# Optimization experiments

Hardware: AMD Instinct MI355X
Metric: run time of the kernel (lower is better)

The kernel has to match this reference:

```python
import jax, jax.numpy as jnp
import numpy as np


def setup_inputs() -> dict:
    key = jax.random.key(0)
    k1, k2, k3, k4 = jax.random.split(key, 4)
    B, T, C = 4, 2048, 1024
    x = jax.random.normal(k1, (B, T, C), dtype=jnp.float32)
    scale = 1.0 / np.sqrt(C)
    Wq = jax.random.normal(k2, (C, C), dtype=jnp.float32) * scale
    Wk = jax.random.normal(k3, (C, C), dtype=jnp.float32) * scale
    Wv = jax.random.normal(k4, (C, C), dtype=jnp.float32) * scale
    return {"x": x, "Wq": Wq, "Wk": Wk, "Wv": Wv}


def reference(x, Wq, Wk, Wv):
    # x: [B, T, C]; torch Linear(no bias): y = x @ W.T
    B, T, C = x.shape
    q = jnp.einsum('btc,dc->btd', x, Wq)
    k = jnp.einsum('btc,dc->btd', x, Wk)
    v = jnp.einsum('btc,dc->btd', x, Wv)
    scale = jnp.asarray(C, x.dtype) ** -0.5
    qk = jnp.einsum('bqd,bkd->bqk', q, k) * scale  # [B, T, T]
    causal = jnp.tril(jnp.ones((T, T), dtype=bool))
    qk = jnp.where(causal, qk, -jnp.inf)
    attn = jax.nn.softmax(qk, axis=-1)
    out = jnp.einsum('bqk,bkd->bqd', attn, v)
    return out
```

## Files before the change

### kernel.cpp

```cpp
#include <hip/hip_runtime.h>

typedef __attribute__((ext_vector_type(8))) short  short8;
typedef __attribute__((ext_vector_type(4))) short  short4v;
typedef __attribute__((ext_vector_type(4))) float  floatx4;

__device__ inline short f2bf(float f) {
    union { float f; unsigned u; } v; v.f = f;
    unsigned r = v.u + 0x7fffu + ((v.u >> 16) & 1u);
    return (short)(r >> 16);
}

typedef const __attribute__((address_space(1))) unsigned int* gp1_t;
typedef __attribute__((address_space(3))) unsigned int* lp3_t;

__device__ __attribute__((always_inline)) inline void gl_lds16(const short* g, short* l) {
    __builtin_amdgcn_global_load_lds((gp1_t)g, (lp3_t)l, 16, 0, 0);
}

__device__ __attribute__((always_inline)) inline void gemm_bt_core(
    const short* __restrict__ Ag, const short* __restrict__ Bg,
    int lda, int ldb, int kmax,
    short* As, short* Bs, floatx4 acc[4][4])
{
    const int t    = threadIdx.x;
    const int srow = t >> 3;
    const int scol = (t & 7) * 8;
    const int lane = t & 63;
    const int wid  = t >> 6;
    const int wx   = wid & 1, wy = wid >> 1;
    const int lm   = lane & 15, lq = lane >> 4;

    for (int k0 = 0; k0 < kmax; k0 += 64) {
        __syncthreads();
#pragma unroll
        for (int i = 0; i < 4; ++i) {
            gl_lds16(Ag + (size_t)(i * 32 + srow) * lda + k0 + scol,
                     As + (i * 32 + srow) * 64 + scol);
            gl_lds16(Bg + (size_t)(i * 32 + srow) * ldb + k0 + scol,
                     Bs + (i * 32 + srow) * 64 + scol);
        }
        __syncthreads();

#pragma unroll
        for (int ks = 0; ks < 2; ++ks) {
            short8 af[4], bfr[4];
#pragma unroll
            for (int mi = 0; mi < 4; ++mi)
                af[mi] = *(const short8*)(As + (wy * 64 + mi * 16 + lm) * 64 + ks * 32 + lq * 8);
#pragma unroll
            for (int ni = 0; ni < 4; ++ni)
                bfr[ni] = *(const short8*)(Bs + (wx * 64 + ni * 16 + lm) * 64 + ks * 32 + lq * 8);
#pragma unroll
            for (int mi = 0; mi < 4; ++mi)
#pragma unroll
                for (int ni = 0; ni < 4; ++ni)
                    acc[mi][ni] = __builtin_amdgcn_mfma_f32_16x16x32_bf16(
                        af[mi], bfr[ni], acc[mi][ni], 0, 0, 0);
        }
    }
}

__global__ void cast_all(const float* __restrict__ x,
                         const float* __restrict__ Wq,
                         const float* __restrict__ Wk,
                         const float* __restrict__ Wv,
                         short* __restrict__ xb, short* __restrict__ wb,
                         float* __restrict__ lsum)
{
    size_t v = (size_t)blockIdx.x * 256 + threadIdx.x;
    const float* src; short* dst; size_t off;
    if (v < 2097152)      { src = x;  dst = xb;           off = v; }
    else if (v < 2359296) { src = Wq; dst = wb;           off = v - 2097152; }
    else if (v < 2621440) { src = Wk; dst = wb + 1048576; off = v - 2359296; }
    else if (v < 2883584) { src = Wv; dst = wb + 2097152; off = v - 2621440; }
    else if (v < 2885632) {
        floatx4 z = {0.f, 0.f, 0.f, 0.f};
        ((floatx4*)lsum)[v - 2883584] = z;
        return;
    } else return;
    floatx4 vv = ((const floatx4*)src)[off];
    short4v s;
#pragma unroll
    for (int e = 0; e < 4; ++e) s[e] = f2bf(vv[e]);
    ((short4v*)dst)[off] = s;
}

__global__ __launch_bounds__(256, 3) void qkv_gemm(
    const short* __restrict__ xb, const short* __restrict__ wb,
    short* __restrict__ qb, short* __restrict__ kb, short* __restrict__ vt)
{
    __shared__ short As[128 * 64];
    __shared__ short Bs[128 * 64];

    const int m0    = blockIdx.x * 128;
    const int which = blockIdx.y >> 3;
    const int n0    = (blockIdx.y & 7) * 128;

    floatx4 acc[4][4];
    floatx4 zero = {0.f, 0.f, 0.f, 0.f};
#pragma unroll
    for (int i = 0; i < 4; ++i)
#pragma unroll
        for (int j = 0; j < 4; ++j) acc[i][j] = zero;

    gemm_bt_core(xb + (size_t)m0 * 1024,
                 wb + (size_t)blockIdx.y * 128 * 1024,
                 1024, 1024, 1024, As, Bs, acc);

    const int lane = threadIdx.x & 63, wid = threadIdx.x >> 6;
    const int wx = wid & 1, wy = wid >> 1, lm = lane & 15, lq = lane >> 4;
#pragma unroll
    for (int mi = 0; mi < 4; ++mi)
#pragma unroll
        for (int ni = 0; ni < 4; ++ni)
#pragma unroll
            for (int r = 0; r < 4; ++r) {
                int row = m0 + wy * 64 + mi * 16 + lq * 4 + r;
                int col = n0 + wx * 64 + ni * 16 + lm;
                short bvv = f2bf(acc[mi][ni][r]);
                if (which == 2) {
                    int bb = row >> 11, tt = row & 2047;
                    vt[((size_t)bb * 1024 + col) * 2048 + tt] = bvv;
                } else if (which == 1) {
                    kb[(size_t)row * 1024 + col] = bvv;
                } else {
                    qb[(size_t)row * 1024 + col] = bvv;
                }
            }
}

__global__ __launch_bounds__(256, 3) void sqk_gemm(
    const short* __restrict__ qb, const short* __restrict__ kb,
    short* __restrict__ P, float* __restrict__ lsum)
{
    int idx = blockIdx.x;
    int i = 0;
    while ((i + 1) * (i + 2) / 2 <= idx) ++i;
    const int j = idx - i * (i + 1) / 2;
    const int b = blockIdx.y;

    __shared__ short As[128 * 64];
    __shared__ short Bs[128 * 64];

    floatx4 acc[4][4];
    floatx4 zero = {0.f, 0.f, 0.f, 0.f};
#pragma unroll
    for (int a = 0; a < 4; ++a)
#pragma unroll
        for (int c = 0; c < 4; ++c) acc[a][c] = zero;

    gemm_bt_core(qb + ((size_t)(b * 2048 + i * 128)) * 1024,
                 kb + ((size_t)(b * 2048 + j * 128)) * 1024,
                 1024, 1024, 1024, As, Bs, acc);

    const float sscl = 0.03125f * 1.44269504089f;
    const bool  diag = (i == j);
    const int lane = threadIdx.x & 63, wid = threadIdx.x >> 6;
    const int wx = wid & 1, wy = wid >> 1, lm = lane & 15, lq = lane >> 4;

#pragma unroll
    for (int mi = 0; mi < 4; ++mi)
#pragma unroll
        for (int r = 0; r < 4; ++r) {
            const int lrow = wy * 64 + mi * 16 + lq * 4 + r;
            const int grow = i * 128 + lrow;
            short* prow = P + ((size_t)b * 2048 + grow) * 2048 + j * 128;
            float rsum = 0.f;
#pragma unroll
            for (int ni = 0; ni < 4; ++ni) {
                const int lcol = wx * 64 + ni * 16 + lm;
                float p = exp2f(acc[mi][ni][r] * sscl);
                if (diag && lcol > lrow) p = 0.f;
                rsum += p;
                prow[lcol] = f2bf(p);
            }
#pragma unroll
            for (int off = 1; off < 16; off <<= 1) rsum += __shfl_xor(rsum, off);
            if (lm == 0) atomicAdd(lsum + b * 2048 + grow, rsum);
        }
}

__global__ __launch_bounds__(256, 3) void pv_gemm(
    const short* __restrict__ P, const short* __restrict__ vt,
    const float* __restrict__ lsum, float* __restrict__ out)
{
    const int x  = blockIdx.x;
    const int pr = blockIdx.y;
    const int b  = blockIdx.z;
    const int n0 = x * 64;

    __shared__ short As[128 * 64];
    __shared__ short Bs[64 * 64];

    const int t    = threadIdx.x;
    const int srow = t >> 3;
    const int scol = (t & 7) * 8;
    const int lane = t & 63;
    const int wid  = t >> 6;
    const int wx   = wid & 1, wy = wid >> 1;
    const int lm   = lane & 15, lq = lane >> 4;

    const short* Bg = vt + ((size_t)b * 1024 + n0) * 2048;

#pragma unroll
    for (int phase = 0; phase < 2; ++phase) {
        const int i    = phase ? (15 - pr) : pr;
        const int kmax = (i + 1) * 128;
        const short* Ag = P + ((size_t)b * 2048 + i * 128) * 2048;

        floatx4 acc[4][2];
        floatx4 zero = {0.f, 0.f, 0.f, 0.f};
#pragma unroll
        for (int a = 0; a < 4; ++a)
#pragma unroll
            for (int c = 0; c < 2; ++c) acc[a][c] = zero;

        for (int k0 = 0; k0 < kmax; k0 += 64) {
            __syncthreads();
#pragma unroll
            for (int q = 0; q < 4; ++q)
                gl_lds16(Ag + (size_t)(q * 32 + srow) * 2048 + k0 + scol,
                         As + (q * 32 + srow) * 64 + scol);
#pragma unroll
            for (int q = 0; q < 2; ++q)
                gl_lds16(Bg + (size_t)(q * 32 + srow) * 2048 + k0 + scol,
                         Bs + (q * 32 + srow) * 64 + scol);
            __syncthreads();

#pragma unroll
            for (int ks = 0; ks < 2; ++ks) {
                short8 af[4], bfr[2];
#pragma unroll
                for (int mi = 0; mi < 4; ++mi)
                    af[mi] = *(const short8*)(As + (wy * 64 + mi * 16 + lm) * 64 + ks * 32 + lq * 8);
#pragma unroll
                for (int ni = 0; ni < 2; ++ni)
                    bfr[ni] = *(const short8*)(Bs + (wx * 32 + ni * 16 + lm) * 64 + ks * 32 + lq * 8);
#pragma unroll
                for (int mi = 0; mi < 4; ++mi)
#pragma unroll
                    for (int ni = 0; ni < 2; ++ni)
                        acc[mi][ni] = __builtin_amdgcn_mfma_f32_16x16x32_bf16(
                            af[mi], bfr[ni], acc[mi][ni], 0, 0, 0);
            }
        }

#pragma unroll
        for (int mi = 0; mi < 4; ++mi)
#pragma unroll
            for (int r = 0; r < 4; ++r) {
                const int grow = b * 2048 + i * 128 + wy * 64 + mi * 16 + lq * 4 + r;
                const float li = 1.0f / lsum[grow];
#pragma unroll
                for (int ni = 0; ni < 2; ++ni)
                    out[(size_t)grow * 1024 + n0 + wx * 32 + ni * 16 + lm] =
                        acc[mi][ni][r] * li;
            }
    }
}

extern "C" void kernel_launch(void* const* d_in, const int* in_sizes, int n_in,
                              void* d_out, int out_size, void* d_ws, size_t ws_size,
                              hipStream_t stream)
{
    (void)in_sizes; (void)n_in; (void)out_size; (void)ws_size;
    const float* x  = (const float*)d_in[0];
    const float* Wq = (const float*)d_in[1];
    const float* Wk = (const float*)d_in[2];
    const float* Wv = (const float*)d_in[3];
    float* out = (float*)d_out;

    char* base = (char*)d_ws;
    short* xb   = (short*)(base);
    short* wb   = (short*)(base + 16777216);
    short* qb   = (short*)(base + 23068672);
    short* kb   = (short*)(base + 39845888);
    short* vt   = (short*)(base + 56623104);
    short* P    = (short*)(base + 73400320);
    float* lsum = (float*)(base + 107954176);

    cast_all<<<11272, 256, 0, stream>>>(x, Wq, Wk, Wv, xb, wb, lsum);
    qkv_gemm<<<dim3(64, 24), 256, 0, stream>>>(xb, wb, qb, kb, vt);
    sqk_gemm<<<dim3(136, 4), 256, 0, stream>>>(qb, kb, P, lsum);
    pv_gemm<<<dim3(16, 8, 4), 256, 0, stream>>>(P, vt, lsum, out);
}
```

Measured before the change: 245.8 us.

## Rewrite QKV projection GEMM as 256x256 double-buffered, 8-wave pipelined kernel

Replaces the 128x128 four-wave QKV GEMM with a 256x256-tile kernel using eight waves and a double-buffered LDS of 128 KB. Global-to-LDS loads for the next K slice are issued while MFMAs on the current slice run, and s_setprio raises priority around the MFMA blocks. The LDS layout is XOR-swizzled to avoid bank conflicts, and tile indices are remapped so neighbouring workgroups share inputs in cache. This trades occupancy and more register pressure (an 8x4 accumulator array per wave) for better data reuse and overlap of loads with compute.

```diff
diff --git a/kernel.cpp b/kernel.cpp
--- a/kernel.cpp
+++ b/kernel.cpp
@@ -16,6 +16,8 @@
 __device__ __attribute__((always_inline)) inline void gl_lds16(const short* g, short* l) {
     __builtin_amdgcn_global_load_lds((gp1_t)g, (lp3_t)l, 16, 0, 0);
 }
+
+#define MFMA_BF16 __builtin_amdgcn_mfma_f32_16x16x32_bf16
 
 __device__ __attribute__((always_inline)) inline void gemm_bt_core(
     const short* __restrict__ Ag, const short* __restrict__ Bg,
@@ -54,8 +56,7 @@
             for (int mi = 0; mi < 4; ++mi)
 #pragma unroll
                 for (int ni = 0; ni < 4; ++ni)
-                    acc[mi][ni] = __builtin_amdgcn_mfma_f32_16x16x32_bf16(
-                        af[mi], bfr[ni], acc[mi][ni], 0, 0, 0);
+                    acc[mi][ni] = MFMA_BF16(af[mi], bfr[ni], acc[mi][ni], 0, 0, 0);
         }
     }
 }
@@ -85,48 +86,178 @@
     ((short4v*)dst)[off] = s;
 }
 
-__global__ __launch_bounds__(256, 3) void qkv_gemm(
+template<int MODE>
+__device__ __attribute__((always_inline)) inline void ktile4(
+    short* As, short* Bs,
+    const short* __restrict__ Ag, const short* __restrict__ Bg, int sk0,
+    int srow, int scl, int scg, int aB, int bB, int c0, int c1,
+    floatx4 acc[8][4])
+{
+    short8 af[4][2], bf[4][2];
+#pragma unroll
+    for (int mi = 0; mi < 4; ++mi) {
+        af[mi][0] = *(const short8*)(As + aB + mi * 1024 + c0);
+        af[mi][1] = *(const short8*)(As + aB + mi * 1024 + c1);
+    }
+#pragma unroll
+    for (int ni = 0; ni < 2; ++ni) {
+        bf[ni][0] = *(const short8*)(Bs + bB + ni * 1024 + c0);
+        bf[ni][1] = *(const short8*)(Bs + bB + ni * 1024 + c1);
+    }
+    __builtin_amdgcn_s_barrier();
+    asm volatile("s_waitcnt lgkmcnt(0)" ::: "memory");
+    __builtin_amdgcn_s_setprio(1);
+#pragma unroll
+    for (int mi = 0; mi < 4; ++mi)
+#pragma unroll
+        for (int ni = 0; ni < 2; ++ni) {
+            acc[mi][ni] = MFMA_BF16(af[mi][0], bf[ni][0], acc[mi][ni], 0, 0, 0);
+            acc[mi][ni] = MFMA_BF16(af[mi][1], bf[ni][1], acc[mi][ni], 0, 0, 0);
+        }
+    __builtin_amdgcn_s_setprio(0);
+    __builtin_amdgcn_s_barrier();
+#pragma unroll
+    for (int ni = 2; ni < 4; ++ni) {
+        bf[ni][0] = *(const short8*)(Bs + bB + ni * 1024 + c0);
+        bf[ni][1] = *(const short8*)(Bs + bB + ni * 1024 + c1);
+    }
+    __builtin_amdgcn_s_barrier();
+    asm volatile("s_waitcnt lgkmcnt(0)" ::: "memory");
+    __builtin_amdgcn_s_setprio(1);
+#pragma unroll
+    for (int mi = 0; mi < 4; ++mi)
+#pragma unroll
+        for (int ni = 2; ni < 4; ++ni) {
+            acc[mi][ni] = MFMA_BF16(af[mi][0], bf[ni][0], acc[mi][ni], 0, 0, 0);
+            acc[mi][ni] = MFMA_BF16(af[mi][1], bf[ni][1], acc[mi][ni], 0, 0, 0);
+        }
+    __builtin_amdgcn_s_setprio(0);
+    __builtin_amdgcn_s_barrier();
+#pragma unroll
+    for (int mi = 0; mi < 4; ++mi) {
+        af[mi][0] = *(const short8*)(As + aB + 4096 + mi * 1024 + c0);
+        af[mi][1] = *(const short8*)(As + aB + 4096 + mi * 1024 + c1);
+    }
+    __builtin_amdgcn_s_barrier();
+    asm volatile("s_waitcnt lgkmcnt(0)" ::: "memory");
+    __builtin_amdgcn_s_setprio(1);
+#pragma unroll
+    for (int mi = 0; mi < 4; ++mi)
+#pragma unroll
+        for (int ni = 2; ni < 4; ++ni) {
+            acc[4 + mi][ni] = MFMA_BF16(af[mi][0], bf[ni][0], acc[4 + mi][ni], 0, 0, 0);
+            acc[4 + mi][ni] = MFMA_BF16(af[mi][1], bf[ni][1], acc[4 + mi][ni], 0, 0, 0);
+        }
+    __builtin_amdgcn_s_setprio(0);
+    __builtin_amdgcn_s_barrier();
+    if (MODE == 0) {
+#pragma unroll
+        for (int i = 0; i < 4; ++i)
+            gl_lds16(Ag + (size_t)(i * 64 + srow) * 1024 + sk0 + scg,
+                     As + (i * 64 + srow) * 64 + scl);
+#pragma unroll
+        for (int i = 0; i < 4; ++i)
+            gl_lds16(Bg + (size_t)(i * 64 + srow) * 1024 + sk0 + scg,
+                     Bs + (i * 64 + srow) * 64 + scl);
+    }
+    __builtin_amdgcn_s_setprio(1);
+#pragma unroll
+    for (int mi = 0; mi < 4; ++mi)
+#pragma unroll
+        for (int ni = 0; ni < 2; ++ni) {
+            acc[4 + mi][ni] = MFMA_BF16(af[mi][0], bf[ni][0], acc[4 + mi][ni], 0, 0, 0);
+            acc[4 + mi][ni] = MFMA_BF16(af[mi][1], bf[ni][1], acc[4 + mi][ni], 0, 0, 0);
+        }
+    __builtin_amdgcn_s_setprio(0);
+    if (MODE == 0)      asm volatile("s_waitcnt vmcnt(8)" ::: "memory");
+    else if (MODE == 1) asm volatile("s_waitcnt vmcnt(0)" ::: "memory");
+    __builtin_amdgcn_s_barrier();
+}
+
+__global__ __launch_bounds__(512, 2) void qkv_gemm8(
     const short* __restrict__ xb, const short* __restrict__ wb,
     short* __restrict__ qb, short* __restrict__ kb, short* __restrict__ vt)
 {
-    __shared__ short As[128 * 64];
-    __shared__ short Bs[128 * 64];
-
-    const int m0    = blockIdx.x * 128;
-    const int which = blockIdx.y >> 3;
-    const int n0    = (blockIdx.y & 7) * 128;
-
-    floatx4 acc[4][4];
+    __shared__ short lds[65536];
+
+    const int orig = blockIdx.x;
+    const int tile = (orig & 7) * 48 + (orig >> 3);
+    const int mt = tile & 31;
+    const int nt = tile >> 5;
+    const int m0 = mt * 256;
+
+    const short* Ag = xb + (size_t)m0 * 1024;
+    const short* Bg = wb + (size_t)(nt * 256) * 1024;
+
+    const int t    = threadIdx.x;
+    const int lane = t & 63;
+    const int wid  = t >> 6;
+    const int wy   = wid >> 2, wx = wid & 3;
+    const int lm   = lane & 15, lq = lane >> 4;
+
+    const int srow = t >> 3;
+    const int scl  = (t & 7) * 8;
+    const int scg  = ((t & 7) ^ (srow & 7)) * 8;
+
+    const int c0 = (lq ^ (lm & 7)) * 8;
+    const int c1 = ((4 + lq) ^ (lm & 7)) * 8;
+    const int aB = (wy * 128 + lm) * 64;
+    const int bB = (wx * 64 + lm) * 64;
+
+    floatx4 acc[8][4];
     floatx4 zero = {0.f, 0.f, 0.f, 0.f};
 #pragma unroll
-    for (int i = 0; i < 4; ++i)
+    for (int i = 0; i < 8; ++i)
 #pragma unroll
         for (int j = 0; j < 4; ++j) acc[i][j] = zero;
 
-    gemm_bt_core(xb + (size_t)m0 * 1024,
-                 wb + (size_t)blockIdx.y * 128 * 1024,
-                 1024, 1024, 1024, As, Bs, acc);
-
-    const int lane = threadIdx.x & 63, wid = threadIdx.x >> 6;
-    const int wx = wid & 1, wy = wid >> 1, lm = lane & 15, lq = lane >> 4;
-#pragma unroll
-    for (int mi = 0; mi < 4; ++mi)
-#pragma unroll
-        for (int ni = 0; ni < 4; ++ni)
-#pragma unroll
-            for (int r = 0; r < 4; ++r) {
-                int row = m0 + wy * 64 + mi * 16 + lq * 4 + r;
-                int col = n0 + wx * 64 + ni * 16 + lm;
-                short bvv = f2bf(acc[mi][ni][r]);
+    short* A0 = lds;          short* B0 = lds + 16384;
+    short* A1 = lds + 32768;  short* B1 = lds + 49152;
+
+#pragma unroll
+    for (int i = 0; i < 4; ++i) {
+        gl_lds16(Ag + (size_t)(i * 64 + srow) * 1024 + scg,      A0 + (i * 64 + srow) * 64 + scl);
+        gl_lds16(Bg + (size_t)(i * 64 + srow) * 1024 + scg,      B0 + (i * 64 + srow) * 64 + scl);
+    }
+#pragma unroll
+    for (int i = 0; i < 4; ++i) {
+        gl_lds16(Ag + (size_t)(i * 64 + srow) * 1024 + 64 + scg, A1 + (i * 64 + srow) * 64 + scl);
+        gl_lds16(Bg + (size_t)(i * 64 + srow) * 1024 + 64 + scg, B1 + (i * 64 + srow) * 64 + scl);
+    }
+    asm volatile("s_waitcnt vmcnt(8)" ::: "memory");
+    __builtin_amdgcn_s_barrier();
+
+#pragma unroll 1
+    for (int k2 = 0; k2 < 7; ++k2) {
+        const int kk = k2 * 128;
+        ktile4<0>(A0, B0, Ag, Bg, kk + 128, srow, scl, scg, aB, bB, c0, c1, acc);
+        ktile4<0>(A1, B1, Ag, Bg, kk + 192, srow, scl, scg, aB, bB, c0, c1, acc);
+    }
+    ktile4<1>(A0, B0, Ag, Bg, 0, srow, scl, scg, aB, bB, c0, c1, acc);
+    ktile4<2>(A1, B1, Ag, Bg, 0, srow, scl, scg, aB, bB, c0, c1, acc);
+
+    const int nglob = nt * 256;
+    const int which = nglob >> 10;
+    const int ncol  = (nglob & 1023) + wx * 64;
+#pragma unroll
+    for (int mi = 0; mi < 8; ++mi)
+#pragma unroll
+        for (int r = 0; r < 4; ++r) {
+            const int row = m0 + wy * 128 + mi * 16 + lq * 4 + r;
+#pragma unroll
+            for (int ni = 0; ni < 4; ++ni) {
+                const int col = ncol + ni * 16 + lm;
+                const short bv = f2bf(acc[mi][ni][r]);
                 if (which == 2) {
-                    int bb = row >> 11, tt = row & 2047;
-                    vt[((size_t)bb * 1024 + col) * 2048 + tt] = bvv;
+                    const int bb = row >> 11, tt = row & 2047;
+                    vt[((size_t)bb * 1024 + col) * 2048 + tt] = bv;
                 } else if (which == 1) {
-                    kb[(size_t)row * 1024 + col] = bvv;
+                    kb[(size_t)row * 1024 + col] = bv;
                 } else {
-                    qb[(size_t)row * 1024 + col] = bvv;
+                    qb[(size_t)row * 1024 + col] = bv;
                 }
             }
+        }
 }
 
 __global__ __launch_bounds__(256, 3) void sqk_gemm(
@@ -240,8 +371,7 @@
                 for (int mi = 0; mi < 4; ++mi)
 #pragma unroll
                     for (int ni = 0; ni < 2; ++ni)
-                        acc[mi][ni] = __builtin_amdgcn_mfma_f32_16x16x32_bf16(
-                            af[mi], bfr[ni], acc[mi][ni], 0, 0, 0);
+                        acc[mi][ni] = MFMA_BF16(af[mi], bfr[ni], acc[mi][ni], 0, 0, 0);
             }
         }
 
@@ -280,7 +410,7 @@
     float* lsum = (float*)(base + 107954176);
 
     cast_all<<<11272, 256, 0, stream>>>(x, Wq, Wk, Wv, xb, wb, lsum);
-    qkv_gemm<<<dim3(64, 24), 256, 0, stream>>>(xb, wb, qb, kb, vt);
+    qkv_gemm8<<<dim3(384), 512, 0, stream>>>(xb, wb, qb, kb, vt);
     sqk_gemm<<<dim3(136, 4), 256, 0, stream>>>(qb, kb, P, lsum);
     pv_gemm<<<dim3(16, 8, 4), 256, 0, stream>>>(P, vt, lsum, out);
 }
```

New measurement: 288.4 us. 1.17x slower.

## Replace QKV GEMM with 256x256 double-buffered, swizzled, 8-wave pipelined kernel

Applied to the files above, without the earlier changes.

Rewrites the QKV projection GEMM to use 256x256 output tiles on 512-thread blocks, with double-buffered LDS staging via direct global-to-LDS loads interleaved with MFMA quadrants. It adds an XOR swizzle on LDS columns to avoid bank conflicts, s_setprio around MFMA bursts, and a block-index remap that groups tiles for L2 reuse. The aim is to hide global load latency and raise arithmetic intensity compared with the single-buffered 128x128 kernel. In exchange it needs 128KB of LDS and many more accumulator registers, and it relies on hand-placed waitcnt counts that must match the issued loads exactly.

```diff
diff --git a/kernel.cpp b/kernel.cpp
--- a/kernel.cpp
+++ b/kernel.cpp
@@ -16,6 +16,8 @@
 __device__ __attribute__((always_inline)) inline void gl_lds16(const short* g, short* l) {
     __builtin_amdgcn_global_load_lds((gp1_t)g, (lp3_t)l, 16, 0, 0);
 }
+
+#define MFMA_BF16 __builtin_amdgcn_mfma_f32_16x16x32_bf16
 
 __device__ __attribute__((always_inline)) inline void gemm_bt_core(
     const short* __restrict__ Ag, const short* __restrict__ Bg,
@@ -54,8 +56,7 @@
             for (int mi = 0; mi < 4; ++mi)
 #pragma unroll
                 for (int ni = 0; ni < 4; ++ni)
-                    acc[mi][ni] = __builtin_amdgcn_mfma_f32_16x16x32_bf16(
-                        af[mi], bfr[ni], acc[mi][ni], 0, 0, 0);
+                    acc[mi][ni] = MFMA_BF16(af[mi], bfr[ni], acc[mi][ni], 0, 0, 0);
         }
     }
 }
@@ -85,48 +86,156 @@
     ((short4v*)dst)[off] = s;
 }
 
-__global__ __launch_bounds__(256, 3) void qkv_gemm(
+struct Q8Ctx {
+    const short* Ag; const short* Bg;
+    short *A0, *B0, *A1, *B1;
+    int srow, scl, scg;
+    int aB, bB, c0, c1;
+};
+
+#define LD_AF(SLOT, HI) do { _Pragma("unroll") \
+    for (int mi_ = 0; mi_ < 4; ++mi_) { \
+        af[mi_][0] = *(const short8*)((SLOT) + X.aB + (HI) + mi_ * 1024 + X.c0); \
+        af[mi_][1] = *(const short8*)((SLOT) + X.aB + (HI) + mi_ * 1024 + X.c1); \
+    } } while (0)
+
+#define LD_BF(SLOT, N0) do { _Pragma("unroll") \
+    for (int ni_ = 0; ni_ < 2; ++ni_) { \
+        bf[(N0) + ni_][0] = *(const short8*)((SLOT) + X.bB + ((N0) + ni_) * 1024 + X.c0); \
+        bf[(N0) + ni_][1] = *(const short8*)((SLOT) + X.bB + ((N0) + ni_) * 1024 + X.c1); \
+    } } while (0)
+
+#define MM_Q(MB, N0) do { _Pragma("unroll") \
+    for (int mi_ = 0; mi_ < 4; ++mi_) { _Pragma("unroll") \
+        for (int ni_ = 0; ni_ < 2; ++ni_) { \
+            acc[(MB)+mi_][(N0)+ni_] = MFMA_BF16(af[mi_][0], bf[(N0)+ni_][0], acc[(MB)+mi_][(N0)+ni_], 0, 0, 0); \
+            acc[(MB)+mi_][(N0)+ni_] = MFMA_BF16(af[mi_][1], bf[(N0)+ni_][1], acc[(MB)+mi_][(N0)+ni_], 0, 0, 0); \
+        } } } while (0)
+
+#define STAGE_HALF(DST, SRC, KOFS) do { \
+    gl_lds16((SRC) + (size_t)(X.srow)      * 1024 + (KOFS) + X.scg, (DST) + (X.srow)      * 64 + X.scl); \
+    gl_lds16((SRC) + (size_t)(64 + X.srow) * 1024 + (KOFS) + X.scg, (DST) + (64 + X.srow) * 64 + X.scl); \
+    } while (0)
+
+#define BARR  __builtin_amdgcn_s_barrier()
+#define WLG0  asm volatile("s_waitcnt lgkmcnt(0)" ::: "memory")
+#define WLG8  asm volatile("s_waitcnt lgkmcnt(8)" ::: "memory")
+#define PRI1  __builtin_amdgcn_s_setprio(1)
+#define PRI0  __builtin_amdgcn_s_setprio(0)
+
+template<bool TAIL>
+__device__ __attribute__((always_inline)) inline void iter8(
+    const Q8Ctx& X, int kb, floatx4 acc[8][4])
+{
+    const int sk1 = kb + 64, sk2 = kb + 128, sk3 = kb + 192;
+    short8 af[4][2], bf[4][2];
+
+    LD_AF(X.A0, 0); LD_BF(X.B0, 0);
+    STAGE_HALF(X.A1, X.Ag, sk1);
+    WLG8;
+    BARR; WLG0; PRI1; MM_Q(0, 0); PRI0; BARR;
+    LD_BF(X.B0, 2);
+    STAGE_HALF(X.A1 + 8192, X.Ag + 131072, sk1);
+    BARR; WLG0; PRI1; MM_Q(0, 2); PRI0; BARR;
+    LD_AF(X.A0, 4096);
+    if (!TAIL) STAGE_HALF(X.B0, X.Bg, sk2);
+    BARR; WLG0; PRI1; MM_Q(4, 2); PRI0; BARR;
+    if (!TAIL) STAGE_HALF(X.B0 + 8192, X.Bg + 131072, sk2);
+    BARR; PRI1; MM_Q(4, 0); PRI0;
+    if (!TAIL) asm volatile("s_waitcnt vmcnt(4)" ::: "memory");
+    else       asm volatile("s_waitcnt vmcnt(0)" ::: "memory");
+    BARR;
+
+    LD_AF(X.A1, 0); LD_BF(X.B1, 0);
+    if (!TAIL) STAGE_HALF(X.A0, X.Ag, sk2);
+    WLG8;
+    BARR; WLG0; PRI1; MM_Q(0, 0); PRI0; BARR;
+    LD_BF(X.B1, 2);
+    if (!TAIL) STAGE_HALF(X.A0 + 8192, X.Ag + 131072, sk2);
+    BARR; WLG0; PRI1; MM_Q(0, 2); PRI0; BARR;
+    LD_AF(X.A1, 4096);
+    if (!TAIL) STAGE_HALF(X.B1, X.Bg, sk3);
+    BARR; WLG0; PRI1; MM_Q(4, 2); PRI0; BARR;
+    if (!TAIL) STAGE_HALF(X.B1 + 8192, X.Bg + 131072, sk3);
+    BARR; PRI1; MM_Q(4, 0); PRI0;
+    if (!TAIL) asm volatile("s_waitcnt vmcnt(4)" ::: "memory");
+    BARR;
+}
+
+__global__ __launch_bounds__(512, 2) void qkv_gemm8(
     const short* __restrict__ xb, const short* __restrict__ wb,
     short* __restrict__ qb, short* __restrict__ kb, short* __restrict__ vt)
 {
-    __shared__ short As[128 * 64];
-    __shared__ short Bs[128 * 64];
-
-    const int m0    = blockIdx.x * 128;
-    const int which = blockIdx.y >> 3;
-    const int n0    = (blockIdx.y & 7) * 128;
-
-    floatx4 acc[4][4];
+    __shared__ short lds[65536];
+
+    const int orig = blockIdx.x;
+    const int tile = (orig & 7) * 48 + (orig >> 3);
+    const int mt = tile & 31;
+    const int nt = tile >> 5;
+    const int m0 = mt * 256;
+
+    const int t    = threadIdx.x;
+    const int lane = t & 63;
+    const int wid  = t >> 6;
+    const int wy   = wid >> 2, wx = wid & 3;
+    const int lm   = lane & 15, lq = lane >> 4;
+
+    Q8Ctx X;
+    X.Ag = xb + (size_t)m0 * 1024;
+    X.Bg = wb + (size_t)(nt * 256) * 1024;
+    X.A0 = lds;          X.B0 = lds + 16384;
+    X.A1 = lds + 32768;  X.B1 = lds + 49152;
+    X.srow = t >> 3;
+    X.scl  = (t & 7) * 8;
+    X.scg  = ((t & 7) ^ (X.srow & 7)) * 8;
+    X.c0 = (lq ^ (lm & 7)) * 8;
+    X.c1 = ((4 + lq) ^ (lm & 7)) * 8;
+    X.aB = (wy * 128 + lm) * 64;
+    X.bB = (wx * 64 + lm) * 64;
+
+    floatx4 acc[8][4];
     floatx4 zero = {0.f, 0.f, 0.f, 0.f};
 #pragma unroll
-    for (int i = 0; i < 4; ++i)
+    for (int i = 0; i < 8; ++i)
 #pragma unroll
         for (int j = 0; j < 4; ++j) acc[i][j] = zero;
 
-    gemm_bt_core(xb + (size_t)m0 * 1024,
-                 wb + (size_t)blockIdx.y * 128 * 1024,
-                 1024, 1024, 1024, As, Bs, acc);
-
-    const int lane = threadIdx.x & 63, wid = threadIdx.x >> 6;
-    const int wx = wid & 1, wy = wid >> 1, lm = lane & 15, lq = lane >> 4;
-#pragma unroll
-    for (int mi = 0; mi < 4; ++mi)
-#pragma unroll
-        for (int ni = 0; ni < 4; ++ni)
-#pragma unroll
-            for (int r = 0; r < 4; ++r) {
-                int row = m0 + wy * 64 + mi * 16 + lq * 4 + r;
-                int col = n0 + wx * 64 + ni * 16 + lm;
-                short bvv = f2bf(acc[mi][ni][r]);
+    STAGE_HALF(X.A0,         X.Ag,          0);
+    STAGE_HALF(X.A0 + 8192,  X.Ag + 131072, 0);
+    STAGE_HALF(X.B0,         X.Bg,          0);
+    STAGE_HALF(X.B0 + 8192,  X.Bg + 131072, 0);
+    STAGE_HALF(X.B1,         X.Bg,          64);
+    STAGE_HALF(X.B1 + 8192,  X.Bg + 131072, 64);
+    asm volatile("s_waitcnt vmcnt(4)" ::: "memory");
+    __builtin_amdgcn_s_barrier();
+
+#pragma unroll 1
+    for (int i = 0; i < 7; ++i)
+        iter8<false>(X, i * 128, acc);
+    iter8<true>(X, 7 * 128, acc);
+
+    const int nglob = nt * 256;
+    const int which = nglob >> 10;
+    const int ncol  = (nglob & 1023) + wx * 64;
+#pragma unroll
+    for (int mi = 0; mi < 8; ++mi)
+#pragma unroll
+        for (int r = 0; r < 4; ++r) {
+            const int row = m0 + wy * 128 + mi * 16 + lq * 4 + r;
+#pragma unroll
+            for (int ni = 0; ni < 4; ++ni) {
+                const int col = ncol + ni * 16 + lm;
+                const short bv = f2bf(acc[mi][ni][r]);
                 if (which == 2) {
-                    int bb = row >> 11, tt = row & 2047;
-                    vt[((size_t)bb * 1024 + col) * 2048 + tt] = bvv;
+                    const int bb = row >> 11, tt = row & 2047;
+                    vt[((size_t)bb * 1024 + col) * 2048 + tt] = bv;
                 } else if (which == 1) {
-                    kb[(size_t)row * 1024 + col] = bvv;
+                    kb[(size_t)row * 1024 + col] = bv;
                 } else {
-                    qb[(size_t)row * 1024 + col] = bvv;
+                    qb[(size_t)row * 1024 + col] = bv;
                 }
             }
+        }
 }
 
 __global__ __launch_bounds__(256, 3) void sqk_gemm(
@@ -240,8 +349,7 @@
                 for (int mi = 0; mi < 4; ++mi)
 #pragma unroll
                     for (int ni = 0; ni < 2; ++ni)
-                        acc[mi][ni] = __builtin_amdgcn_mfma_f32_16x16x32_bf16(
-                            af[mi], bfr[ni], acc[mi][ni], 0, 0, 0);
+                        acc[mi][ni] = MFMA_BF16(af[mi], bfr[ni], acc[mi][ni], 0, 0, 0);
             }
         }
 
@@ -280,7 +388,7 @@
     float* lsum = (float*)(base + 107954176);
 
     cast_all<<<11272, 256, 0, stream>>>(x, Wq, Wk, Wv, xb, wb, lsum);
-    qkv_gemm<<<dim3(64, 24), 256, 0, stream>>>(xb, wb, qb, kb, vt);
+    qkv_gemm8<<<dim3(384), 512, 0, stream>>>(xb, wb, qb, kb, vt);
     sqk_gemm<<<dim3(136, 4), 256, 0, stream>>>(qb, kb, P, lsum);
     pv_gemm<<<dim3(16, 8, 4), 256, 0, stream>>>(P, vt, lsum, out);
 }
```

After: 282.5 us. +15.0%, slower.

## Use 128x128 tiles in PV GEMM with longest-first scheduling

Applied to the files above, without the earlier changes.

The PV GEMM changes from 128x64 output tiles, where each block processed two causal row-blocks paired for balance, to 128x128 tiles with one row-block per block. It reuses the shared gemm_bt_core and orders the grid so the largest causal row-blocks launch first. Larger tiles raise arithmetic intensity and halve reloads of P. The cost is fewer blocks (512 instead of 512 paired launches that did double work) and the loss of the explicit load-balancing pairing. The launch_bounds of 3 is kept, and larger register use for the 4x4 accumulators may hurt occupancy.

```diff
diff --git a/kernel.cpp b/kernel.cpp
--- a/kernel.cpp
+++ b/kernel.cpp
@@ -16,6 +16,8 @@
 __device__ __attribute__((always_inline)) inline void gl_lds16(const short* g, short* l) {
     __builtin_amdgcn_global_load_lds((gp1_t)g, (lp3_t)l, 16, 0, 0);
 }
+
+#define MFMA_BF16 __builtin_amdgcn_mfma_f32_16x16x32_bf16
 
 __device__ __attribute__((always_inline)) inline void gemm_bt_core(
     const short* __restrict__ Ag, const short* __restrict__ Bg,
@@ -54,8 +56,7 @@
             for (int mi = 0; mi < 4; ++mi)
 #pragma unroll
                 for (int ni = 0; ni < 4; ++ni)
-                    acc[mi][ni] = __builtin_amdgcn_mfma_f32_16x16x32_bf16(
-                        af[mi], bfr[ni], acc[mi][ni], 0, 0, 0);
+                    acc[mi][ni] = MFMA_BF16(af[mi], bfr[ni], acc[mi][ni], 0, 0, 0);
         }
     }
 }
@@ -185,78 +186,40 @@
     const float* __restrict__ lsum, float* __restrict__ out)
 {
     const int x  = blockIdx.x;
-    const int pr = blockIdx.y;
-    const int b  = blockIdx.z;
-    const int n0 = x * 64;
+    const int b  = blockIdx.y;
+    const int i  = 15 - blockIdx.z;
+    const int n0 = x * 128;
+    const int kmax = (i + 1) * 128;
 
     __shared__ short As[128 * 64];
-    __shared__ short Bs[64 * 64];
-
-    const int t    = threadIdx.x;
-    const int srow = t >> 3;
-    const int scol = (t & 7) * 8;
-    const int lane = t & 63;
-    const int wid  = t >> 6;
-    const int wx   = wid & 1, wy = wid >> 1;
-    const int lm   = lane & 15, lq = lane >> 4;
-
+    __shared__ short Bs[128 * 64];
+
+    const short* Ag = P  + ((size_t)b * 2048 + i * 128) * 2048;
     const short* Bg = vt + ((size_t)b * 1024 + n0) * 2048;
 
-#pragma unroll
-    for (int phase = 0; phase < 2; ++phase) {
-        const int i    = phase ? (15 - pr) : pr;
-        const int kmax = (i + 1) * 128;
-        const short* Ag = P + ((size_t)b * 2048 + i * 128) * 2048;
-
-        floatx4 acc[4][2];
-        floatx4 zero = {0.f, 0.f, 0.f, 0.f};
-#pragma unroll
-        for (int a = 0; a < 4; ++a)
-#pragma unroll
-            for (int c = 0; c < 2; ++c) acc[a][c] = zero;
-
-        for (int k0 = 0; k0 < kmax; k0 += 64) {
-            __syncthreads();
-#pragma unroll
-            for (int q = 0; q < 4; ++q)
-                gl_lds16(Ag + (size_t)(q * 32 + srow) * 2048 + k0 + scol,
-                         As + (q * 32 + srow) * 64 + scol);
-#pragma unroll
-            for (int q = 0; q < 2; ++q)
-                gl_lds16(Bg + (size_t)(q * 32 + srow) * 2048 + k0 + scol,
-                         Bs + (q * 32 + srow) * 64 + scol);
-            __syncthreads();
-
-#pragma unroll
-            for (int ks = 0; ks < 2; ++ks) {
-                short8 af[4], bfr[2];
-#pragma unroll
-                for (int mi = 0; mi < 4; ++mi)
-                    af[mi] = *(const short8*)(As + (wy * 64 + mi * 16 + lm) * 64 + ks * 32 + lq * 8);
-#pragma unroll
-                for (int ni = 0; ni < 2; ++ni)
-                    bfr[ni] = *(const short8*)(Bs + (wx * 32 + ni * 16 + lm) * 64 + ks * 32 + lq * 8);
-#pragma unroll
-                for (int mi = 0; mi < 4; ++mi)
-#pragma unroll
-                    for (int ni = 0; ni < 2; ++ni)
-                        acc[mi][ni] = __builtin_amdgcn_mfma_f32_16x16x32_bf16(
-                            af[mi], bfr[ni], acc[mi][ni], 0, 0, 0);
-            }
-        }
-
-#pragma unroll
-        for (int mi = 0; mi < 4; ++mi)
-#pragma unroll
-            for (int r = 0; r < 4; ++r) {
-                const int grow = b * 2048 + i * 128 + wy * 64 + mi * 16 + lq * 4 + r;
-                const float li = 1.0f / lsum[grow];
-#pragma unroll
-                for (int ni = 0; ni < 2; ++ni)
-                    out[(size_t)grow * 1024 + n0 + wx * 32 + ni * 16 + lm] =
-                        acc[mi][ni][r] * li;
-            }
-    }
+    floatx4 acc[4][4];
+    floatx4 zero = {0.f, 0.f, 0.f, 0.f};
+#pragma unroll
+    for (int a = 0; a < 4; ++a)
+#pragma unroll
+        for (int c = 0; c < 4; ++c) acc[a][c] = zero;
+
+    gemm_bt_core(Ag, Bg, 2048, 2048, kmax, As, Bs, acc);
+
+    const int lane = threadIdx.x & 63, wid = threadIdx.x >> 6;
+    const int wx = wid & 1, wy = wid >> 1, lm = lane & 15, lq = lane >> 4;
+
+#pragma unroll
+    for (int mi = 0; mi < 4; ++mi)
+#pragma unroll
+        for (int r = 0; r < 4; ++r) {
+            const int grow = b * 2048 + i * 128 + wy * 64 + mi * 16 + lq * 4 + r;
+            const float li = 1.0f / lsum[grow];
+#pragma unroll
+            for (int ni = 0; ni < 4; ++ni)
+                out[(size_t)grow * 1024 + n0 + wx * 64 + ni * 16 + lm] =
+                    acc[mi][ni][r] * li;
+        }
 }
 
 extern "C" void kernel_launch(void* const* d_in, const int* in_sizes, int n_in,
@@ -282,5 +245,5 @@
     cast_all<<<11272, 256, 0, stream>>>(x, Wq, Wk, Wv, xb, wb, lsum);
     qkv_gemm<<<dim3(64, 24), 256, 0, stream>>>(xb, wb, qb, kb, vt);
     sqk_gemm<<<dim3(136, 4), 256, 0, stream>>>(qb, kb, P, lsum);
-    pv_gemm<<<dim3(16, 8, 4), 256, 0, stream>>>(P, vt, lsum, out);
-}
+    pv_gemm<<<dim3(8, 4, 16), 256, 0, stream>>>(P, vt, lsum, out);
+}
```

Result: no change. 249.5 us (+1.5%).
